# Performance work log

Hardware: AMD Instinct MI355X
Metric: run time of the kernel (lower is better)

The kernel has to match this reference:

```python
import jax, jax.numpy as jnp
import numpy as np

E = 384      # dim_embd
H = 6        # n_heads
D = E // H   # head dim = 64
T_MAX = 256  # block_size
EPS = 1e-5


def setup_inputs() -> dict:
    key = jax.random.key(0)
    ks = jax.random.split(key, 12)
    B, T = 128, 256
    s_in = (1.0 / E) ** 0.5
    s_ff = (1.0 / (4 * E)) ** 0.5
    return {
        "x": jax.random.normal(ks[0], (B, T, E), jnp.float32),
        # per-head projections stacked to match torch concat order: [E, H*D]
        "wq": jax.random.normal(ks[1], (E, E), jnp.float32) * s_in,
        "wk": jax.random.normal(ks[2], (E, E), jnp.float32) * s_in,
        "wv": jax.random.normal(ks[3], (E, E), jnp.float32) * s_in,
        "w_proj": jax.random.normal(ks[4], (E, E), jnp.float32) * s_in,
        "b_proj": jnp.zeros((E,), jnp.float32),
        "w1": jax.random.normal(ks[5], (E, 4 * E), jnp.float32) * s_in,
        "b1": jnp.zeros((4 * E,), jnp.float32),
        "w2": jax.random.normal(ks[6], (4 * E, E), jnp.float32) * s_ff,
        "b2": jnp.zeros((E,), jnp.float32),
        "g1": jnp.ones((E,), jnp.float32),
        "beta1": jnp.zeros((E,), jnp.float32),
        "g2": jnp.ones((E,), jnp.float32),
        "beta2": jnp.zeros((E,), jnp.float32),
    }


def _layernorm(x, g, b):
    mu = jnp.mean(x, axis=-1, keepdims=True)
    var = jnp.mean(jnp.square(x - mu), axis=-1, keepdims=True)
    return (x - mu) * jax.lax.rsqrt(var + EPS) * g + b


def _attention(x, wq, wk, wv, w_proj, b_proj):
    B, T, C = x.shape
    # batched per-head projections: [B,T,H,D]
    q = (x @ wq).reshape(B, T, H, D)
    k = (x @ wk).reshape(B, T, H, D)
    v = (x @ wv).reshape(B, T, H, D)
    # NOTE: original scales by C**-0.5 with C = full embed dim (384)
    scale = C ** (-0.5)
    scores = jnp.einsum("bthd,bshd->bhts", q, k) * scale
    mask = jnp.tril(jnp.ones((T, T), bool))
    scores = jnp.where(mask, scores, -jnp.inf)
    wei = jax.nn.softmax(scores, axis=-1)  # dropout = identity (eval)
    out = jnp.einsum("bhts,bshd->bthd", wei, v).reshape(B, T, C)
    return out @ w_proj + b_proj


def reference(x, wq, wk, wv, w_proj, b_proj, w1, b1, w2, b2, g1, beta1, g2, beta2):
    x = x + _attention(_layernorm(x, g1, beta1), wq, wk, wv, w_proj, b_proj)
    h = _layernorm(x, g2, beta2)
    h = jax.nn.relu(h @ w1 + b1) @ w2 + b2  # dropout = identity (eval)
    return x + h
```

## Files before the change

kernel.cpp:

```cpp
#include <hip/hip_runtime.h>
#include <hip/hip_bf16.h>

typedef __attribute__((ext_vector_type(8))) short bf16x8;
typedef __attribute__((ext_vector_type(4))) float f32x4;

#define MFMA_BF16(a, b, c) __builtin_amdgcn_mfma_f32_16x16x32_bf16((a), (b), (c), 0, 0, 0)

#define E_DIM 384
#define T_SEQ 256
#define B_BATCH 128
#define H_HEADS 6
#define D_HEAD 64
#define NROWS (B_BATCH * T_SEQ)
#define FF_DIM (4 * E_DIM)
#define QKV_LD 1152

__device__ __forceinline__ void load_lds16(const __hip_bfloat16* g, __hip_bfloat16* l) {
    __builtin_amdgcn_global_load_lds(
        (const __attribute__((address_space(1))) void*)g,
        (__attribute__((address_space(3))) void*)l, 16, 0, 0);
}

__device__ __forceinline__ float to_f(float x) { return x; }
__device__ __forceinline__ float to_f(__hip_bfloat16 x) { return __bfloat162float(x); }

__global__ void tcast_all_kernel(const float* __restrict__ wq, const float* __restrict__ wk,
                                 const float* __restrict__ wv, const float* __restrict__ wp,
                                 const float* __restrict__ w1, const float* __restrict__ w2,
                                 __hip_bfloat16* __restrict__ wqkvT, __hip_bfloat16* __restrict__ wpT,
                                 __hip_bfloat16* __restrict__ w1T, __hip_bfloat16* __restrict__ w2T) {
    const int WE = E_DIM * E_DIM;
    const int FE = E_DIM * FF_DIM;
    int idx = blockIdx.x * 256 + threadIdx.x;
    if (idx < 3 * WE) {
        int seg = idx / WE, j = idx - seg * WE;
        const float* W = seg == 0 ? wq : (seg == 1 ? wk : wv);
        int k = j / E_DIM, n = j - k * E_DIM;
        wqkvT[(size_t)seg * WE + (size_t)n * E_DIM + k] = __float2bfloat16(W[j]);
    } else if (idx < 4 * WE) {
        int j = idx - 3 * WE;
        int k = j / E_DIM, n = j - k * E_DIM;
        wpT[(size_t)n * E_DIM + k] = __float2bfloat16(wp[j]);
    } else if (idx < 4 * WE + FE) {
        int j = idx - 4 * WE;
        int k = j / FF_DIM, n = j - k * FF_DIM;
        w1T[(size_t)n * E_DIM + k] = __float2bfloat16(w1[j]);
    } else {
        int j = idx - 4 * WE - FE;
        int k = j / E_DIM, n = j - k * E_DIM;
        w2T[(size_t)n * FF_DIM + k] = __float2bfloat16(w2[j]);
    }
}

template <typename TI>
__global__ __launch_bounds__(256) void ln_kernel(const TI* __restrict__ x,
                                                 const float* __restrict__ g,
                                                 const float* __restrict__ bta,
                                                 __hip_bfloat16* __restrict__ out) {
    int row = blockIdx.x * 4 + (threadIdx.x >> 6);
    int lane = threadIdx.x & 63;
    const TI* xr = x + (size_t)row * E_DIM;
    float vals[6];
    float s = 0.f;
#pragma unroll
    for (int i = 0; i < 6; i++) {
        vals[i] = to_f(xr[lane + i * 64]);
        s += vals[i];
    }
#pragma unroll
    for (int off = 1; off < 64; off <<= 1) s += __shfl_xor(s, off, 64);
    float mu = s * (1.f / E_DIM);
    float vv = 0.f;
#pragma unroll
    for (int i = 0; i < 6; i++) {
        float d = vals[i] - mu;
        vv += d * d;
    }
#pragma unroll
    for (int off = 1; off < 64; off <<= 1) vv += __shfl_xor(vv, off, 64);
    float rstd = rsqrtf(vv * (1.f / E_DIM) + 1e-5f);
#pragma unroll
    for (int i = 0; i < 6; i++) {
        int c = lane + i * 64;
        out[(size_t)row * E_DIM + c] =
            __float2bfloat16((vals[i] - mu) * rstd * g[c] + bta[c]);
    }
}

template <int EPI, int NW>
__global__ __launch_bounds__(NW * 64, NW == 8 ? 4 : 3) void gemm_kernel(
    const __hip_bfloat16* __restrict__ A, const __hip_bfloat16* __restrict__ BT,
    const float* __restrict__ bias, const void* __restrict__ resid,
    void* __restrict__ outp, int M, int N, int K) {
    constexpr int BM = NW * 32;
    constexpr int T = NW * 64;
    constexpr int BUF = (BM + 128) * 32;
    __shared__ __hip_bfloat16 lds[3 * BUF];
    const int t = threadIdx.x;
    const int w = t >> 6, lane = t & 63;
    const int l16 = lane & 15, lhi = lane >> 4;
    const int wm = w >> 1, wn = w & 1;

    const int nwg = gridDim.x;
    const int bid = blockIdx.x;
    const int cpx = nwg >> 3;
    const int swz = (bid & 7) * cpx + (bid >> 3);
    const int nb = N >> 7;
    const int m0 = (swz / nb) * BM;
    const int n0 = (swz % nb) * 128;

    const int ql = (t & 7) ^ ((t >> 3) & 7);
    const int sr = 2 * (t >> 3) + (ql >> 2);
    const int scol = (ql & 3) * 8;
    const __hip_bfloat16* pa0 = A + (size_t)(m0 + sr) * K + scol;
    const __hip_bfloat16* pa1 = pa0 + (size_t)(T / 4) * K;
    const __hip_bfloat16* pb0 = BT + (size_t)(n0 + sr) * K + scol;
    const __hip_bfloat16* pb1 = pb0 + (size_t)(T / 4) * K;
    const int dstA = t * 8;

    int aoff[4], boff[4];
#pragma unroll
    for (int mr = 0; mr < 4; mr++) {
        int R = wm * 64 + mr * 16 + l16;
        int L = R >> 1;
        int q = (((R & 1) << 2) | lhi) ^ (L & 7);
        aoff[mr] = L * 64 + q * 8;
    }
#pragma unroll
    for (int nr = 0; nr < 4; nr++) {
        int R = wn * 64 + nr * 16 + l16;
        int L = R >> 1;
        int q = (((R & 1) << 2) | lhi) ^ (L & 7);
        boff[nr] = BM * 32 + L * 64 + q * 8;
    }

    f32x4 acc[4][4] = {};
    const int nk = K >> 5;

#define STAGE(sbuf)                                                           \
    {                                                                         \
        __hip_bfloat16* sb_ = &lds[(sbuf) * BUF];                             \
        load_lds16(pa0, sb_ + dstA);                                          \
        load_lds16(pa1, sb_ + T * 8 + dstA);                                  \
        load_lds16(pb0, sb_ + BM * 32 + dstA);                                \
        if constexpr (NW == 4) load_lds16(pb1, sb_ + BM * 32 + T * 8 + dstA); \
        pa0 += 32;                                                            \
        pa1 += 32;                                                            \
        pb0 += 32;                                                            \
        if constexpr (NW == 4) pb1 += 32;                                     \
    }

    STAGE(0);
    STAGE(1);
    int rb = 0, sbx = 2;

    for (int kt = 0; kt < nk; kt++) {
        if (kt + 1 < nk) {
            if constexpr (NW == 8) asm volatile("s_waitcnt vmcnt(3)" ::: "memory");
            else                   asm volatile("s_waitcnt vmcnt(4)" ::: "memory");
        } else {
            asm volatile("s_waitcnt vmcnt(0)" ::: "memory");
        }
        __builtin_amdgcn_s_barrier();
        __builtin_amdgcn_sched_barrier(0);
        if (kt + 2 < nk) STAGE(sbx);
        const __hip_bfloat16* base = &lds[rb * BUF];
        bf16x8 af[4], bg[4];
#pragma unroll
        for (int mr = 0; mr < 4; mr++)
            af[mr] = *reinterpret_cast<const bf16x8*>(base + aoff[mr]);
#pragma unroll
        for (int nr = 0; nr < 4; nr++)
            bg[nr] = *reinterpret_cast<const bf16x8*>(base + boff[nr]);
        __builtin_amdgcn_s_setprio(1);
#pragma unroll
        for (int mr = 0; mr < 4; mr++)
#pragma unroll
            for (int nr = 0; nr < 4; nr++)
                acc[mr][nr] = MFMA_BF16(af[mr], bg[nr], acc[mr][nr]);
        __builtin_amdgcn_s_setprio(0);
        rb = rb == 2 ? 0 : rb + 1;
        sbx = sbx == 2 ? 0 : sbx + 1;
    }
#undef STAGE

    __hip_bfloat16* outb = (__hip_bfloat16*)outp;
    float* outf = (float*)outp;
#pragma unroll
    for (int mr = 0; mr < 4; mr++) {
#pragma unroll
        for (int nr = 0; nr < 4; nr++) {
            const int col = n0 + wn * 64 + nr * 16 + l16;
#pragma unroll
            for (int r = 0; r < 4; r++) {
                const int row = m0 + wm * 64 + mr * 16 + lhi * 4 + r;
                const size_t off = (size_t)row * N + col;
                float v = acc[mr][nr][r];
                if (EPI == 0) {
                    outb[off] = __float2bfloat16(v);
                } else if (EPI == 2) {
                    v += bias[col];
                    outb[off] = __float2bfloat16(v > 0.f ? v : 0.f);
                } else if (EPI == 3) {
                    v += bias[col] + ((const float*)resid)[off];
                    outb[off] = __float2bfloat16(v);
                } else {
                    v += bias[col] + to_f(((const __hip_bfloat16*)resid)[off]);
                    outf[off] = v;
                }
            }
        }
    }
}

__global__ __launch_bounds__(512, 1) void attn_kernel(
    const __hip_bfloat16* __restrict__ qkv, __hip_bfloat16* __restrict__ o) {
    __shared__ __hip_bfloat16 Ks[T_SEQ][72];
    __shared__ __hip_bfloat16 VTs[D_HEAD][264];
    __shared__ __hip_bfloat16 Ps[8][32][72];

    const int bh = blockIdx.x;
    const int b = bh / H_HEADS, h = bh - b * H_HEADS;
    const int t = threadIdx.x;
    const int w = t >> 6, lane = t & 63;
    const int l16 = lane & 15, lhi = lane >> 4;
    const size_t rbase = (size_t)b * T_SEQ;
    const int qoff = h * D_HEAD, koff = E_DIM + h * D_HEAD, voff = 2 * E_DIM + h * D_HEAD;
    const float qscale = 0.051031036307982884f * 1.4426950408889634f;

    bf16x8 qf[2][2];
#pragma unroll
    for (int mr = 0; mr < 2; mr++)
#pragma unroll
        for (int kk = 0; kk < 2; kk++)
            qf[mr][kk] = *reinterpret_cast<const bf16x8*>(
                qkv + (rbase + w * 32 + mr * 16 + l16) * QKV_LD + qoff + kk * 32 + lhi * 8);

#pragma unroll
    for (int i = 0; i < 4; i++) {
        int idx = i * 512 + t;
        int r = idx >> 3, c = (idx & 7) * 8;
        *reinterpret_cast<uint4*>(&Ks[r][c]) =
            *reinterpret_cast<const uint4*>(qkv + (rbase + r) * QKV_LD + koff + c);
    }
#pragma unroll
    for (int i = 0; i < 4; i++) {
        int idx = i * 512 + t;
        int r = idx >> 3, d0 = (idx & 7) * 8;
        uint4 val = *reinterpret_cast<const uint4*>(qkv + (rbase + r) * QKV_LD + voff + d0);
        const __hip_bfloat16* p8 = reinterpret_cast<const __hip_bfloat16*>(&val);
#pragma unroll
        for (int j = 0; j < 8; j++) VTs[d0 + j][r] = p8[j];
    }
    __syncthreads();

    float mstate[2][4], lstate[2][4];
    f32x4 oacc[2][4] = {};
#pragma unroll
    for (int mr = 0; mr < 2; mr++)
#pragma unroll
        for (int r = 0; r < 4; r++) {
            mstate[mr][r] = -1e30f;
            lstate[mr][r] = 0.f;
        }

    const int njt = (w >> 1) + 1;
    for (int jt = 0; jt < njt; jt++) {
        const bool diag = (jt == (w >> 1));
        f32x4 s[2][4] = {};
#pragma unroll
        for (int kk = 0; kk < 2; kk++) {
            bf16x8 kf[4];
#pragma unroll
            for (int nr = 0; nr < 4; nr++)
                kf[nr] = *reinterpret_cast<const bf16x8*>(
                    &Ks[jt * 64 + nr * 16 + l16][kk * 32 + lhi * 8]);
#pragma unroll
            for (int mr = 0; mr < 2; mr++)
#pragma unroll
                for (int nr = 0; nr < 4; nr++)
                    s[mr][nr] = MFMA_BF16(qf[mr][kk], kf[nr], s[mr][nr]);
        }
#pragma unroll
        for (int mr = 0; mr < 2; mr++) {
#pragma unroll
            for (int r = 0; r < 4; r++) {
                int qrow = w * 32 + mr * 16 + lhi * 4 + r;
                float pv[4];
                float mx = -1e30f;
                if (diag) {
#pragma unroll
                    for (int nr = 0; nr < 4; nr++) {
                        int kcol = jt * 64 + nr * 16 + l16;
                        float val = s[mr][nr][r] * qscale;
                        if (kcol > qrow) val = -1e30f;
                        pv[nr] = val;
                        mx = fmaxf(mx, val);
                    }
                } else {
#pragma unroll
                    for (int nr = 0; nr < 4; nr++) {
                        float val = s[mr][nr][r] * qscale;
                        pv[nr] = val;
                        mx = fmaxf(mx, val);
                    }
                }
#pragma unroll
                for (int off = 1; off < 16; off <<= 1)
                    mx = fmaxf(mx, __shfl_xor(mx, off, 64));
                float mold = mstate[mr][r];
                float mnew = fmaxf(mold, mx);
                float corr = exp2f(mold - mnew);
                float psum = 0.f;
#pragma unroll
                for (int nr = 0; nr < 4; nr++) {
                    float p = exp2f(pv[nr] - mnew);
                    pv[nr] = p;
                    psum += p;
                }
#pragma unroll
                for (int off = 1; off < 16; off <<= 1)
                    psum += __shfl_xor(psum, off, 64);
                lstate[mr][r] = lstate[mr][r] * corr + psum;
                mstate[mr][r] = mnew;
#pragma unroll
                for (int dr = 0; dr < 4; dr++) oacc[mr][dr][r] *= corr;
#pragma unroll
                for (int nr = 0; nr < 4; nr++)
                    Ps[w][mr * 16 + lhi * 4 + r][nr * 16 + l16] = __float2bfloat16(pv[nr]);
            }
        }
#pragma unroll
        for (int kk = 0; kk < 2; kk++) {
            bf16x8 pa[2], vbf[4];
#pragma unroll
            for (int mr = 0; mr < 2; mr++)
                pa[mr] = *reinterpret_cast<const bf16x8*>(
                    &Ps[w][mr * 16 + l16][kk * 32 + lhi * 8]);
#pragma unroll
            for (int dr = 0; dr < 4; dr++)
                vbf[dr] = *reinterpret_cast<const bf16x8*>(
                    &VTs[dr * 16 + l16][jt * 64 + kk * 32 + lhi * 8]);
#pragma unroll
            for (int mr = 0; mr < 2; mr++)
#pragma unroll
                for (int dr = 0; dr < 4; dr++)
                    oacc[mr][dr] = MFMA_BF16(pa[mr], vbf[dr], oacc[mr][dr]);
        }
    }

#pragma unroll
    for (int mr = 0; mr < 2; mr++) {
#pragma unroll
        for (int r = 0; r < 4; r++) {
            float rl = 1.f / lstate[mr][r];
            int row = w * 32 + mr * 16 + lhi * 4 + r;
#pragma unroll
            for (int dr = 0; dr < 4; dr++)
                o[(rbase + row) * E_DIM + h * D_HEAD + dr * 16 + l16] =
                    __float2bfloat16(oacc[mr][dr][r] * rl);
        }
    }
}

extern "C" void kernel_launch(void* const* d_in, const int* in_sizes, int n_in,
                              void* d_out, int out_size, void* d_ws, size_t ws_size,
                              hipStream_t stream) {
    const float* x      = (const float*)d_in[0];
    const float* wq     = (const float*)d_in[1];
    const float* wk     = (const float*)d_in[2];
    const float* wv     = (const float*)d_in[3];
    const float* w_proj = (const float*)d_in[4];
    const float* b_proj = (const float*)d_in[5];
    const float* w1     = (const float*)d_in[6];
    const float* b1     = (const float*)d_in[7];
    const float* w2     = (const float*)d_in[8];
    const float* b2     = (const float*)d_in[9];
    const float* g1     = (const float*)d_in[10];
    const float* bt1    = (const float*)d_in[11];
    const float* g2     = (const float*)d_in[12];
    const float* bt2    = (const float*)d_in[13];
    float* out = (float*)d_out;

    char* ws = (char*)d_ws;
    size_t off = 0;
    auto alloc = [&](size_t bytes) {
        void* p = ws + off;
        off += (bytes + 255) & ~(size_t)255;
        return p;
    };
    const size_t wElems = E_DIM * E_DIM;
    const size_t fElems = E_DIM * FF_DIM;
    const size_t actElems = (size_t)NROWS * E_DIM;
    __hip_bfloat16* wqkvT = (__hip_bfloat16*)alloc(3 * wElems * 2);
    __hip_bfloat16* wpT   = (__hip_bfloat16*)alloc(wElems * 2);
    __hip_bfloat16* w1T   = (__hip_bfloat16*)alloc(fElems * 2);
    __hip_bfloat16* w2T   = (__hip_bfloat16*)alloc(fElems * 2);
    __hip_bfloat16* lnb   = (__hip_bfloat16*)alloc(actElems * 2);
    __hip_bfloat16* x2b   = (__hip_bfloat16*)alloc(actElems * 2);
    __hip_bfloat16* qkv   = (__hip_bfloat16*)alloc(3 * actElems * 2);
    __hip_bfloat16* ab    = (__hip_bfloat16*)alloc(actElems * 2);
    __hip_bfloat16* h1    = qkv;

    tcast_all_kernel<<<6912, 256, 0, stream>>>(wq, wk, wv, w_proj, w1, w2,
                                               wqkvT, wpT, w1T, w2T);

    ln_kernel<float><<<NROWS / 4, 256, 0, stream>>>(x, g1, bt1, lnb);

    gemm_kernel<0, 8><<<(NROWS / 256) * (QKV_LD / 128), 512, 0, stream>>>(
        lnb, wqkvT, nullptr, nullptr, qkv, NROWS, QKV_LD, E_DIM);

    attn_kernel<<<B_BATCH * H_HEADS, 512, 0, stream>>>(qkv, ab);

    gemm_kernel<3, 4><<<(NROWS / 128) * (E_DIM / 128), 256, 0, stream>>>(
        ab, wpT, b_proj, x, x2b, NROWS, E_DIM, E_DIM);

    ln_kernel<__hip_bfloat16><<<NROWS / 4, 256, 0, stream>>>(x2b, g2, bt2, lnb);

    gemm_kernel<2, 8><<<(NROWS / 256) * (FF_DIM / 128), 512, 0, stream>>>(
        lnb, w1T, b1, nullptr, h1, NROWS, FF_DIM, E_DIM);

    gemm_kernel<4, 4><<<(NROWS / 128) * (E_DIM / 128), 256, 0, stream>>>(
        h1, w2T, b2, x2b, out, NROWS, E_DIM, FF_DIM);
}
```

Before: 247.9 us.

## Rebalance causal attention across 4 waves, swizzle LDS, vectorize layernorm

The attention kernel now runs 4 waves per block, and each wave handles two complementary query chunks (c and 7-c), which evens out the causal work per wave and allows two blocks per CU. K is loaded directly into LDS with global_load_lds, and K, V^T and P use XOR-swizzled layouts instead of padding to avoid bank conflicts. LayerNorm uses 2-wide vector loads and stores, and the QKV GEMM switches to the 4-wave tile config. The risks are a register-heavy unrolled two-pass loop and V-transpose scatter stores.

```diff
diff --git a/kernel.cpp b/kernel.cpp
--- a/kernel.cpp
+++ b/kernel.cpp
@@ -63,9 +63,20 @@
     float vals[6];
     float s = 0.f;
 #pragma unroll
-    for (int i = 0; i < 6; i++) {
-        vals[i] = to_f(xr[lane + i * 64]);
-        s += vals[i];
+    for (int i = 0; i < 3; i++) {
+        int c = i * 128 + 2 * lane;
+        if constexpr (sizeof(TI) == 4) {
+            float2 v = *reinterpret_cast<const float2*>(&xr[c]);
+            vals[2 * i] = v.x;
+            vals[2 * i + 1] = v.y;
+        } else {
+            ushort2 u = *reinterpret_cast<const ushort2*>(&xr[c]);
+            union { unsigned short us; __hip_bfloat16 h; } a, b2;
+            a.us = u.x; b2.us = u.y;
+            vals[2 * i] = __bfloat162float(a.h);
+            vals[2 * i + 1] = __bfloat162float(b2.h);
+        }
+        s += vals[2 * i] + vals[2 * i + 1];
     }
 #pragma unroll
     for (int off = 1; off < 64; off <<= 1) s += __shfl_xor(s, off, 64);
@@ -80,10 +91,14 @@
     for (int off = 1; off < 64; off <<= 1) vv += __shfl_xor(vv, off, 64);
     float rstd = rsqrtf(vv * (1.f / E_DIM) + 1e-5f);
 #pragma unroll
-    for (int i = 0; i < 6; i++) {
-        int c = lane + i * 64;
-        out[(size_t)row * E_DIM + c] =
-            __float2bfloat16((vals[i] - mu) * rstd * g[c] + bta[c]);
+    for (int i = 0; i < 3; i++) {
+        int c = i * 128 + 2 * lane;
+        float2 gv = *reinterpret_cast<const float2*>(&g[c]);
+        float2 bv = *reinterpret_cast<const float2*>(&bta[c]);
+        union { ushort2 u; struct { __hip_bfloat16 a, b; } h; } o2;
+        o2.h.a = __float2bfloat16((vals[2 * i] - mu) * rstd * gv.x + bv.x);
+        o2.h.b = __float2bfloat16((vals[2 * i + 1] - mu) * rstd * gv.y + bv.y);
+        *reinterpret_cast<ushort2*>(&out[(size_t)row * E_DIM + c]) = o2.u;
     }
 }
 
@@ -213,152 +228,173 @@
     }
 }
 
-__global__ __launch_bounds__(512, 1) void attn_kernel(
+__global__ __launch_bounds__(256, 2) void attn_kernel(
     const __hip_bfloat16* __restrict__ qkv, __hip_bfloat16* __restrict__ o) {
-    __shared__ __hip_bfloat16 Ks[T_SEQ][72];
-    __shared__ __hip_bfloat16 VTs[D_HEAD][264];
-    __shared__ __hip_bfloat16 Ps[8][32][72];
+    __shared__ __hip_bfloat16 Ks[T_SEQ * 64];
+    __shared__ __hip_bfloat16 VTs[64 * 256];
+    __shared__ __hip_bfloat16 Ps[4 * 2048];
 
     const int bh = blockIdx.x;
     const int b = bh / H_HEADS, h = bh - b * H_HEADS;
     const int t = threadIdx.x;
     const int w = t >> 6, lane = t & 63;
     const int l16 = lane & 15, lhi = lane >> 4;
+    const int l8 = l16 & 7;
     const size_t rbase = (size_t)b * T_SEQ;
     const int qoff = h * D_HEAD, koff = E_DIM + h * D_HEAD, voff = 2 * E_DIM + h * D_HEAD;
     const float qscale = 0.051031036307982884f * 1.4426950408889634f;
 
-    bf16x8 qf[2][2];
-#pragma unroll
-    for (int mr = 0; mr < 2; mr++)
-#pragma unroll
-        for (int kk = 0; kk < 2; kk++)
-            qf[mr][kk] = *reinterpret_cast<const bf16x8*>(
-                qkv + (rbase + w * 32 + mr * 16 + l16) * QKV_LD + qoff + kk * 32 + lhi * 8);
-
-#pragma unroll
-    for (int i = 0; i < 4; i++) {
-        int idx = i * 512 + t;
-        int r = idx >> 3, c = (idx & 7) * 8;
-        *reinterpret_cast<uint4*>(&Ks[r][c]) =
-            *reinterpret_cast<const uint4*>(qkv + (rbase + r) * QKV_LD + koff + c);
-    }
-#pragma unroll
-    for (int i = 0; i < 4; i++) {
-        int idx = i * 512 + t;
+#pragma unroll
+    for (int i = 0; i < 8; i++) {
+        int idx = i * 256 + t;
+        int r = idx >> 3;
+        int c8 = idx & 7;
+        load_lds16(qkv + (rbase + r) * QKV_LD + koff + ((c8 ^ (r & 7)) << 3),
+                   &Ks[idx * 8]);
+    }
+#pragma unroll
+    for (int i = 0; i < 8; i++) {
+        int idx = i * 256 + t;
         int r = idx >> 3, d0 = (idx & 7) * 8;
         uint4 val = *reinterpret_cast<const uint4*>(qkv + (rbase + r) * QKV_LD + voff + d0);
         const __hip_bfloat16* p8 = reinterpret_cast<const __hip_bfloat16*>(&val);
-#pragma unroll
-        for (int j = 0; j < 8; j++) VTs[d0 + j][r] = p8[j];
+        int slot = r >> 3, rin = r & 7;
+#pragma unroll
+        for (int j = 0; j < 8; j++) {
+            int d = d0 + j;
+            VTs[d * 256 + ((slot ^ (d & 7)) << 3) + rin] = p8[j];
+        }
     }
     __syncthreads();
 
-    float mstate[2][4], lstate[2][4];
-    f32x4 oacc[2][4] = {};
-#pragma unroll
-    for (int mr = 0; mr < 2; mr++)
-#pragma unroll
-        for (int r = 0; r < 4; r++) {
-            mstate[mr][r] = -1e30f;
-            lstate[mr][r] = 0.f;
-        }
-
-    const int njt = (w >> 1) + 1;
-    for (int jt = 0; jt < njt; jt++) {
-        const bool diag = (jt == (w >> 1));
-        f32x4 s[2][4] = {};
-#pragma unroll
-        for (int kk = 0; kk < 2; kk++) {
-            bf16x8 kf[4];
-#pragma unroll
-            for (int nr = 0; nr < 4; nr++)
-                kf[nr] = *reinterpret_cast<const bf16x8*>(
-                    &Ks[jt * 64 + nr * 16 + l16][kk * 32 + lhi * 8]);
-#pragma unroll
-            for (int mr = 0; mr < 2; mr++)
-#pragma unroll
-                for (int nr = 0; nr < 4; nr++)
-                    s[mr][nr] = MFMA_BF16(qf[mr][kk], kf[nr], s[mr][nr]);
-        }
-#pragma unroll
-        for (int mr = 0; mr < 2; mr++) {
+#pragma unroll
+    for (int cp = 0; cp < 2; cp++) {
+        const int c = cp ? 7 - w : w;
+        bf16x8 qf[2][2];
+#pragma unroll
+        for (int mr = 0; mr < 2; mr++)
+#pragma unroll
+            for (int kk = 0; kk < 2; kk++)
+                qf[mr][kk] = *reinterpret_cast<const bf16x8*>(
+                    qkv + (rbase + c * 32 + mr * 16 + l16) * QKV_LD + qoff + kk * 32 + lhi * 8);
+
+        float mstate[2][4], lstate[2][4];
+        f32x4 oacc[2][4] = {};
+#pragma unroll
+        for (int mr = 0; mr < 2; mr++)
 #pragma unroll
             for (int r = 0; r < 4; r++) {
-                int qrow = w * 32 + mr * 16 + lhi * 4 + r;
-                float pv[4];
-                float mx = -1e30f;
-                if (diag) {
+                mstate[mr][r] = -1e30f;
+                lstate[mr][r] = 0.f;
+            }
+
+        const int njt = (c >> 1) + 1;
+        for (int jt = 0; jt < njt; jt++) {
+            const bool diag = (jt == (c >> 1));
+            f32x4 s[2][4] = {};
+#pragma unroll
+            for (int kk = 0; kk < 2; kk++) {
+                bf16x8 kf[4];
+#pragma unroll
+                for (int nr = 0; nr < 4; nr++) {
+                    int R = jt * 64 + nr * 16 + l16;
+                    kf[nr] = *reinterpret_cast<const bf16x8*>(
+                        &Ks[R * 64 + (((kk << 2) + lhi) ^ l8) * 8]);
+                }
+#pragma unroll
+                for (int mr = 0; mr < 2; mr++)
+#pragma unroll
+                    for (int nr = 0; nr < 4; nr++)
+                        s[mr][nr] = MFMA_BF16(qf[mr][kk], kf[nr], s[mr][nr]);
+            }
+#pragma unroll
+            for (int mr = 0; mr < 2; mr++) {
+#pragma unroll
+                for (int r = 0; r < 4; r++) {
+                    int qrow = c * 32 + mr * 16 + lhi * 4 + r;
+                    float pv[4];
+                    float mx = -1e30f;
+                    if (diag) {
+#pragma unroll
+                        for (int nr = 0; nr < 4; nr++) {
+                            int kcol = jt * 64 + nr * 16 + l16;
+                            float val = s[mr][nr][r] * qscale;
+                            if (kcol > qrow) val = -1e30f;
+                            pv[nr] = val;
+                            mx = fmaxf(mx, val);
+                        }
+                    } else {
+#pragma unroll
+                        for (int nr = 0; nr < 4; nr++) {
+                            float val = s[mr][nr][r] * qscale;
+                            pv[nr] = val;
+                            mx = fmaxf(mx, val);
+                        }
+                    }
+#pragma unroll
+                    for (int off = 1; off < 16; off <<= 1)
+                        mx = fmaxf(mx, __shfl_xor(mx, off, 64));
+                    float mold = mstate[mr][r];
+                    float mnew = fmaxf(mold, mx);
+                    float corr = exp2f(mold - mnew);
+                    float psum = 0.f;
 #pragma unroll
                     for (int nr = 0; nr < 4; nr++) {
-                        int kcol = jt * 64 + nr * 16 + l16;
-                        float val = s[mr][nr][r] * qscale;
-                        if (kcol > qrow) val = -1e30f;
-                        pv[nr] = val;
-                        mx = fmaxf(mx, val);
+                        float p = exp2f(pv[nr] - mnew);
+                        pv[nr] = p;
+                        psum += p;
                     }
-                } else {
+#pragma unroll
+                    for (int off = 1; off < 16; off <<= 1)
+                        psum += __shfl_xor(psum, off, 64);
+                    lstate[mr][r] = lstate[mr][r] * corr + psum;
+                    mstate[mr][r] = mnew;
+#pragma unroll
+                    for (int dr = 0; dr < 4; dr++) oacc[mr][dr][r] *= corr;
+                    int pr = mr * 16 + lhi * 4 + r;
 #pragma unroll
                     for (int nr = 0; nr < 4; nr++) {
-                        float val = s[mr][nr][r] * qscale;
-                        pv[nr] = val;
-                        mx = fmaxf(mx, val);
+                        int slot = (nr << 1) + (l16 >> 3);
+                        Ps[w * 2048 + pr * 64 + ((slot ^ (pr & 7)) << 3) + l8] =
+                            __float2bfloat16(pv[nr]);
                     }
                 }
-#pragma unroll
-                for (int off = 1; off < 16; off <<= 1)
-                    mx = fmaxf(mx, __shfl_xor(mx, off, 64));
-                float mold = mstate[mr][r];
-                float mnew = fmaxf(mold, mx);
-                float corr = exp2f(mold - mnew);
-                float psum = 0.f;
-#pragma unroll
-                for (int nr = 0; nr < 4; nr++) {
-                    float p = exp2f(pv[nr] - mnew);
-                    pv[nr] = p;
-                    psum += p;
+            }
+#pragma unroll
+            for (int kk = 0; kk < 2; kk++) {
+                bf16x8 pa[2], vbf[4];
+#pragma unroll
+                for (int mr = 0; mr < 2; mr++) {
+                    int row = mr * 16 + l16;
+                    pa[mr] = *reinterpret_cast<const bf16x8*>(
+                        &Ps[w * 2048 + row * 64 + (((kk << 2) + lhi) ^ l8) * 8]);
                 }
 #pragma unroll
-                for (int off = 1; off < 16; off <<= 1)
-                    psum += __shfl_xor(psum, off, 64);
-                lstate[mr][r] = lstate[mr][r] * corr + psum;
-                mstate[mr][r] = mnew;
-#pragma unroll
-                for (int dr = 0; dr < 4; dr++) oacc[mr][dr][r] *= corr;
-#pragma unroll
-                for (int nr = 0; nr < 4; nr++)
-                    Ps[w][mr * 16 + lhi * 4 + r][nr * 16 + l16] = __float2bfloat16(pv[nr]);
-            }
-        }
-#pragma unroll
-        for (int kk = 0; kk < 2; kk++) {
-            bf16x8 pa[2], vbf[4];
-#pragma unroll
-            for (int mr = 0; mr < 2; mr++)
-                pa[mr] = *reinterpret_cast<const bf16x8*>(
-                    &Ps[w][mr * 16 + l16][kk * 32 + lhi * 8]);
-#pragma unroll
-            for (int dr = 0; dr < 4; dr++)
-                vbf[dr] = *reinterpret_cast<const bf16x8*>(
-                    &VTs[dr * 16 + l16][jt * 64 + kk * 32 + lhi * 8]);
-#pragma unroll
-            for (int mr = 0; mr < 2; mr++)
+                for (int dr = 0; dr < 4; dr++) {
+                    int d = dr * 16 + l16;
+                    int slot = (jt << 3) + (kk << 2) + lhi;
+                    vbf[dr] = *reinterpret_cast<const bf16x8*>(
+                        &VTs[d * 256 + ((slot ^ l8) << 3)]);
+                }
+#pragma unroll
+                for (int mr = 0; mr < 2; mr++)
+#pragma unroll
+                    for (int dr = 0; dr < 4; dr++)
+                        oacc[mr][dr] = MFMA_BF16(pa[mr], vbf[dr], oacc[mr][dr]);
+            }
+        }
+
+#pragma unroll
+        for (int mr = 0; mr < 2; mr++) {
+#pragma unroll
+            for (int r = 0; r < 4; r++) {
+                float rl = 1.f / lstate[mr][r];
+                int row = c * 32 + mr * 16 + lhi * 4 + r;
 #pragma unroll
                 for (int dr = 0; dr < 4; dr++)
-                    oacc[mr][dr] = MFMA_BF16(pa[mr], vbf[dr], oacc[mr][dr]);
-        }
-    }
-
-#pragma unroll
-    for (int mr = 0; mr < 2; mr++) {
-#pragma unroll
-        for (int r = 0; r < 4; r++) {
-            float rl = 1.f / lstate[mr][r];
-            int row = w * 32 + mr * 16 + lhi * 4 + r;
-#pragma unroll
-            for (int dr = 0; dr < 4; dr++)
-                o[(rbase + row) * E_DIM + h * D_HEAD + dr * 16 + l16] =
-                    __float2bfloat16(oacc[mr][dr][r] * rl);
+                    o[(rbase + row) * E_DIM + h * D_HEAD + dr * 16 + l16] =
+                        __float2bfloat16(oacc[mr][dr][r] * rl);
+            }
         }
     }
 }
@@ -407,10 +443,10 @@
 
     ln_kernel<float><<<NROWS / 4, 256, 0, stream>>>(x, g1, bt1, lnb);
 
-    gemm_kernel<0, 8><<<(NROWS / 256) * (QKV_LD / 128), 512, 0, stream>>>(
+    gemm_kernel<0, 4><<<(NROWS / 128) * (QKV_LD / 128), 256, 0, stream>>>(
         lnb, wqkvT, nullptr, nullptr, qkv, NROWS, QKV_LD, E_DIM);
 
-    attn_kernel<<<B_BATCH * H_HEADS, 512, 0, stream>>>(qkv, ab);
+    attn_kernel<<<B_BATCH * H_HEADS, 256, 0, stream>>>(qkv, ab);
 
     gemm_kernel<3, 4><<<(NROWS / 128) * (E_DIM / 128), 256, 0, stream>>>(
         ab, wpT, b_proj, x, x2b, NROWS, E_DIM, E_DIM);
```

New measurement: 248.7 us. About the same (+0.3%).
